# Kernel tuning notes

Measured on AMD Instinct MI355X. Metric: run time of the kernel, lower is better.

Reference implementation:

```python
import jax, jax.numpy as jnp
import numpy as np

GAMMA = 1.0
EPS = 1e-8


def setup_inputs() -> dict:
    key = jax.random.key(0)
    k1, k2 = jax.random.split(key)
    inputs = jax.random.normal(k1, (16, 2048, 1024), dtype=jnp.float32)
    codebook = jax.random.normal(k2, (2048, 1024), dtype=jnp.float32)  # normal(1.0) init
    return {"inputs": inputs, "codebook": codebook}


def reference(inputs, codebook):
    # inputs: [B, T, D]; codebook: [K, D]
    features = jax.lax.stop_gradient(inputs)
    # similarity = sum over D of features[..., None, :] * codebook -> [B, T, K]
    similarity = jnp.einsum('btd,kd->btk', features, codebook)
    scores = jax.nn.softmax(similarity, axis=-1)  # [B, T, K]
    nn_idx = jnp.argmax(scores, axis=-1)  # [B, T]
    # one_hot(nn_idx) @ codebook == direct gather
    quantized = codebook[nn_idx]  # [B, T, D]
    quantized = quantized - jnp.mean(quantized, axis=-1, keepdims=True)
    quantized = quantized / jnp.linalg.norm(quantized, axis=-1, keepdims=True)
    # entropy loss
    flat = scores.reshape(-1, scores.shape[-1])  # [B*T, K]
    h_clust = -jnp.mean(jnp.sum(flat * jnp.log2(flat + EPS), axis=-1))
    diversity = jnp.mean(flat, axis=0)  # [K]
    h_diversity = -jnp.sum(diversity * jnp.log2(diversity + EPS))
    loss = h_clust - GAMMA * h_diversity
    quantization_loss = jnp.full(scores.shape, loss)  # [B, T, K], scalar broadcast
    # straight-through estimator
    quantized = inputs + jax.lax.stop_gradient(quantized - inputs)
    return (quantized, quantization_loss, nn_idx, codebook)
```

## Files before the change

### kernel.cpp

```cpp
#include <hip/hip_runtime.h>
#include <math.h>

#define M_TOTAL 32768
#define D_DIM   1024
#define K_DIM   2048

#define OUT0_OFF 0ULL
#define OUT1_OFF 33554432ULL
#define OUT2_OFF 100663296ULL
#define OUT3_OFF 100696064ULL

typedef _Float16 f16x4 __attribute__((ext_vector_type(4)));
typedef _Float16 f16x8 __attribute__((ext_vector_type(8)));
typedef float    f32x4 __attribute__((ext_vector_type(4)));

#define STR_(x) #x
#define STR(x) STR_(x)
#define WAITVM(N) asm volatile("s_waitcnt vmcnt(" STR(N) ")" ::: "memory")

__device__ __forceinline__ void async_copy16(void* lds, const void* g) {
    __builtin_amdgcn_global_load_lds(
        (const __attribute__((address_space(1))) unsigned int*)g,
        (__attribute__((address_space(3))) unsigned int*)lds, 16, 0, 0);
}

__global__ __launch_bounds__(256) void convcb_kernel(const float* __restrict__ C,
                                                     _Float16* __restrict__ ch,
                                                     _Float16* __restrict__ cl) {
    const int i = blockIdx.x * 256 + threadIdx.x;
    const float4 c = ((const float4*)C)[i];
    f16x4 h, l;
    h.x = (_Float16)c.x; l.x = (_Float16)(c.x - (float)h.x);
    h.y = (_Float16)c.y; l.y = (_Float16)(c.y - (float)h.y);
    h.z = (_Float16)c.z; l.z = (_Float16)(c.z - (float)h.z);
    h.w = (_Float16)c.w; l.w = (_Float16)(c.w - (float)h.w);
    ((f16x4*)ch)[i] = h;
    ((f16x4*)cl)[i] = l;
}

__global__ __launch_bounds__(256) void convx_kernel(const float* __restrict__ X,
                                                    _Float16* __restrict__ xh) {
    const size_t i = (size_t)blockIdx.x * 256 + threadIdx.x;
    const float4 a = ((const float4*)X)[i];
    f16x4 h;
    h.x = (_Float16)a.x; h.y = (_Float16)a.y;
    h.z = (_Float16)a.z; h.w = (_Float16)a.w;
    ((f16x4*)xh)[i] = h;
}

__device__ __forceinline__ void loadA4(f16x8* a, const _Float16* Ab, int wm, int fr, int fq, int kh) {
#pragma unroll
    for (int mi = 0; mi < 4; mi++) {
        const int row = wm + mi * 16 + fr;
        a[mi] = *(const f16x8*)(Ab + kh * 8192 + row * 32 + (fq ^ ((row >> 1) & 3)) * 8);
    }
}
__device__ __forceinline__ void loadB4(f16x8* b, const _Float16* Bb, int wn, int fr, int fq, int kh) {
#pragma unroll
    for (int ni = 0; ni < 4; ni++) {
        const int row = wn + ni * 16 + fr;
        b[ni] = *(const f16x8*)(Bb + kh * 4096 + row * 32 + (fq ^ ((row >> 1) & 3)) * 8);
    }
}

__global__ __launch_bounds__(512) void gemm_kernel(const _Float16* __restrict__ XH,
                                                   const _Float16* __restrict__ CH,
                                                   const _Float16* __restrict__ CL,
                                                   float* __restrict__ S) {
    __shared__ _Float16 lds[65536];
    _Float16* const A0  = lds;
    _Float16* const Bh0 = lds + 16384;
    _Float16* const Bl0 = lds + 24576;
    _Float16* const A1  = lds + 32768;
    _Float16* const Bh1 = lds + 49152;
    _Float16* const Bl1 = lds + 57344;

    const int tid  = threadIdx.x;
    const int lane = tid & 63;
    const int wave = tid >> 6;

    const int bq  = blockIdx.x;
    const int xcd = bq & 7;
    const int idx = bq >> 3;
    const int m0 = (xcd * 16 + (idx >> 4)) * 256;
    const int n0 = (idx & 15) * 128;

    const int wm = (wave & 3) * 64;
    const int wn = (wave >> 2) * 64;
    const int fr = lane & 15;
    const int fq = lane >> 4;

    size_t aoff[2][2]; int alds[2][2];
#pragma unroll
    for (int e = 0; e < 2; e++) {
        const int U = (wave * 2 + e) * 64 + lane;
        const int row = U >> 2;
#pragma unroll
        for (int kh = 0; kh < 2; kh++) {
            aoff[e][kh] = (size_t)(m0 + row) * D_DIM + (size_t)(kh * 4 + ((U & 3) ^ ((row >> 1) & 3))) * 8;
            alds[e][kh] = kh * 8192 + (wave * 2 + e) * 512;
        }
    }
    size_t boff[2]; int blds[2];
    {
        const int U = wave * 64 + lane;
        const int row = U >> 2;
#pragma unroll
        for (int kh = 0; kh < 2; kh++) {
            boff[kh] = (size_t)(n0 + row) * D_DIM + (size_t)(kh * 4 + ((U & 3) ^ ((row >> 1) & 3))) * 8;
            blds[kh] = kh * 4096 + wave * 512;
        }
    }

#define STAGE_A(Abuf, KH, kb) do {                                                        \
    async_copy16((void*)((Abuf) + alds[0][KH]), (const void*)(XH + aoff[0][KH] + (kb)));  \
    async_copy16((void*)((Abuf) + alds[1][KH]), (const void*)(XH + aoff[1][KH] + (kb)));  \
} while (0)
#define STAGE_BH(Bbuf, KH, kb) async_copy16((void*)((Bbuf) + blds[KH]), (const void*)(CH + boff[KH] + (kb)))
#define STAGE_BL(Bbuf, KH, kb) async_copy16((void*)((Bbuf) + blds[KH]), (const void*)(CL + boff[KH] + (kb)))

#define PH_MFMA() do {                                                                    \
    __builtin_amdgcn_s_barrier();                                                         \
    asm volatile("s_waitcnt lgkmcnt(0)" ::: "memory");                                    \
    __builtin_amdgcn_sched_barrier(0);                                                    \
    __builtin_amdgcn_s_setprio(1);                                                        \
    _Pragma("unroll")                                                                     \
    for (int mi = 0; mi < 4; mi++) {                                                      \
        _Pragma("unroll")                                                                 \
        for (int ni = 0; ni < 4; ni++)                                                    \
            acc[mi][ni] = __builtin_amdgcn_mfma_f32_16x16x32_f16(a[mi], b[ni], acc[mi][ni], 0, 0, 0); \
    }                                                                                     \
    __builtin_amdgcn_s_setprio(0);                                                        \
    __builtin_amdgcn_s_barrier();                                                         \
} while (0)

    f32x4 acc[4][4];
#pragma unroll
    for (int mi = 0; mi < 4; mi++)
#pragma unroll
        for (int ni = 0; ni < 4; ni++) {
            acc[mi][ni].x = 0.f; acc[mi][ni].y = 0.f;
            acc[mi][ni].z = 0.f; acc[mi][ni].w = 0.f;
        }

    f16x8 a[4], b[4];

    STAGE_A(A0, 0, 0); STAGE_BH(Bh0, 0, 0);
    STAGE_BL(Bl0, 0, 0);
    STAGE_A(A0, 1, 0); STAGE_BH(Bh0, 1, 0);
    STAGE_BL(Bl0, 1, 0);
    WAITVM(5);
    __builtin_amdgcn_s_barrier();

    for (int t = 0; t < 15; t++) {
        _Float16* const Ac  = (t & 1) ? A1 : A0;
        _Float16* const Bhc = (t & 1) ? Bh1 : Bh0;
        _Float16* const Blc = (t & 1) ? Bl1 : Bl0;
        _Float16* const An  = (t & 1) ? A0 : A1;
        _Float16* const Bhn = (t & 1) ? Bh0 : Bh1;
        _Float16* const Bln = (t & 1) ? Bl0 : Bl1;
        const size_t kb = (size_t)(t + 1) * 64;

        loadA4(a, Ac, wm, fr, fq, 0);
        loadB4(b, Bhc, wn, fr, fq, 0);
        STAGE_A(An, 0, kb); STAGE_BH(Bhn, 0, kb);
        WAITVM(7);
        PH_MFMA();
        loadB4(b, Blc, wn, fr, fq, 0);
        STAGE_BL(Bln, 0, kb);
        WAITVM(5);
        PH_MFMA();
        loadA4(a, Ac, wm, fr, fq, 1);
        loadB4(b, Bhc, wn, fr, fq, 1);
        STAGE_A(An, 1, kb); STAGE_BH(Bhn, 1, kb);
        WAITVM(7);
        PH_MFMA();
        loadB4(b, Blc, wn, fr, fq, 1);
        STAGE_BL(Bln, 1, kb);
        WAITVM(5);
        PH_MFMA();
    }

    loadA4(a, A1, wm, fr, fq, 0);
    loadB4(b, Bh1, wn, fr, fq, 0);
    WAITVM(4);
    PH_MFMA();
    loadB4(b, Bl1, wn, fr, fq, 0);
    WAITVM(1);
    PH_MFMA();
    loadA4(a, A1, wm, fr, fq, 1);
    loadB4(b, Bh1, wn, fr, fq, 1);
    WAITVM(0);
    PH_MFMA();
    loadB4(b, Bl1, wn, fr, fq, 1);
    __builtin_amdgcn_s_barrier();
    asm volatile("s_waitcnt lgkmcnt(0)" ::: "memory");
    __builtin_amdgcn_sched_barrier(0);
#pragma unroll
    for (int mi = 0; mi < 4; mi++)
#pragma unroll
        for (int ni = 0; ni < 4; ni++)
            acc[mi][ni] = __builtin_amdgcn_mfma_f32_16x16x32_f16(a[mi], b[ni], acc[mi][ni], 0, 0, 0);

#pragma unroll
    for (int mi = 0; mi < 4; mi++)
#pragma unroll
        for (int r = 0; r < 4; r++) {
            float* dst = S + (size_t)(m0 + wm + mi * 16 + fq * 4 + r) * K_DIM + n0 + wn;
#pragma unroll
            for (int ni = 0; ni < 4; ni++) dst[ni * 16 + fr] = acc[mi][ni][r];
        }
#undef STAGE_A
#undef STAGE_BH
#undef STAGE_BL
#undef PH_MFMA
}

#define MARGIN 0.125f
__global__ __launch_bounds__(256) void rowstats_kernel(const float* __restrict__ S,
                                                       int* __restrict__ cnt,
                                                       int* __restrict__ cand,
                                                       float* __restrict__ div_acc,
                                                       float* __restrict__ hclust_acc) {
    __shared__ float sdiv[K_DIM];
    const int tid = threadIdx.x;
    for (int k = tid; k < K_DIM; k += 256) sdiv[k] = 0.0f;
    __syncthreads();

    const int lane = tid & 63;
    const int wave = tid >> 6;

    float dreg[32];
#pragma unroll
    for (int j = 0; j < 32; j++) dreg[j] = 0.0f;
    float ent_acc = 0.0f;

    for (int r8 = 0; r8 < 8; r8++) {
        const int row = blockIdx.x * 32 + wave * 8 + r8;
        const float* srow = S + (size_t)row * K_DIM;

        float v[32];
#pragma unroll
        for (int j = 0; j < 32; j++) v[j] = srow[lane + 64 * j];

        float m = v[0];
#pragma unroll
        for (int j = 1; j < 32; j++) m = fmaxf(m, v[j]);
        for (int off = 32; off > 0; off >>= 1) m = fmaxf(m, __shfl_xor(m, off, 64));

        const float thresh = m - MARGIN;
#pragma unroll
        for (int j = 0; j < 32; j++) {
            if (v[j] > thresh) {
                const int slot = atomicAdd(&cnt[row], 1);
                if (slot < 8) cand[row * 8 + slot] = lane + 64 * j;
            }
        }

        float Z = 0.0f;
#pragma unroll
        for (int j = 0; j < 32; j++) {
            v[j] = __expf(v[j] - m);
            Z += v[j];
        }
        for (int off = 32; off > 0; off >>= 1) Z += __shfl_xor(Z, off, 64);
        const float invZ = 1.0f / Z;

#pragma unroll
        for (int j = 0; j < 32; j++) {
            const float p = v[j] * invZ;
            dreg[j] += p;
            ent_acc += p * __log2f(p + 1e-8f);
        }
    }

#pragma unroll
    for (int j = 0; j < 32; j++) atomicAdd(&sdiv[lane + 64 * j], dreg[j]);
    for (int off = 32; off > 0; off >>= 1) ent_acc += __shfl_xor(ent_acc, off, 64);
    if (lane == 0) atomicAdd(hclust_acc, ent_acc);
    __syncthreads();

    for (int k = tid; k < K_DIM; k += 256) atomicAdd(&div_acc[k], sdiv[k]);
}

__global__ __launch_bounds__(256) void refineq_kernel(const float* __restrict__ X,
                                                      const float* __restrict__ C,
                                                      const int* __restrict__ cnt,
                                                      const int* __restrict__ cand,
                                                      float* __restrict__ nn_out,
                                                      float* __restrict__ out0) {
    const int tid = threadIdx.x;
    const int lane = tid & 63;
    const int wave = tid >> 6;
    const int row = blockIdx.x * 4 + wave;

    const int n = min(cnt[row], 8);
    const float* x = X + (size_t)row * D_DIM;

    float4 xv[4];
#pragma unroll
    for (int q = 0; q < 4; q++) xv[q] = *(const float4*)(x + lane * 4 + 256 * q);

    double bestv = -1.0e300;
    int besti = 0x7fffffff;
    for (int c = 0; c < n; c++) {
        const int idx = cand[row * 8 + c];
        const float* cb = C + (size_t)idx * D_DIM;
        double s = 0.0;
#pragma unroll
        for (int q = 0; q < 4; q++) {
            const float4 cv = *(const float4*)(cb + lane * 4 + 256 * q);
            s += (double)xv[q].x * cv.x + (double)xv[q].y * cv.y +
                 (double)xv[q].z * cv.z + (double)xv[q].w * cv.w;
        }
        for (int off = 32; off > 0; off >>= 1) s += __shfl_xor(s, off, 64);
        if (s > bestv || (s == bestv && idx < besti)) { bestv = s; besti = idx; }
    }
    if (lane == 0) nn_out[row] = (float)besti;

    const float* c = C + (size_t)besti * D_DIM;
    float4 v[4];
    float sum = 0.0f;
#pragma unroll
    for (int q = 0; q < 4; q++) {
        v[q] = *(const float4*)(c + lane * 4 + 256 * q);
        sum += v[q].x + v[q].y + v[q].z + v[q].w;
    }
    for (int off = 32; off > 0; off >>= 1) sum += __shfl_xor(sum, off, 64);
    const float mean = sum * (1.0f / 1024.0f);

    float ss = 0.0f;
#pragma unroll
    for (int q = 0; q < 4; q++) {
        v[q].x -= mean; v[q].y -= mean; v[q].z -= mean; v[q].w -= mean;
        ss += v[q].x * v[q].x + v[q].y * v[q].y + v[q].z * v[q].z + v[q].w * v[q].w;
    }
    for (int off = 32; off > 0; off >>= 1) ss += __shfl_xor(ss, off, 64);
    const float inv = 1.0f / sqrtf(ss);

    float* o = out0 + (size_t)row * D_DIM;
#pragma unroll
    for (int q = 0; q < 4; q++) {
        float4 w = v[q];
        w.x *= inv; w.y *= inv; w.z *= inv; w.w *= inv;
        *(float4*)(o + lane * 4 + 256 * q) = w;
    }
}

__global__ __launch_bounds__(256) void finalize_kernel(const float* __restrict__ div_acc,
                                                       const float* __restrict__ hclust_acc,
                                                       float* __restrict__ loss_out) {
    __shared__ float red[256];
    const int tid = threadIdx.x;
    float sum = 0.0f;
    for (int k = tid; k < K_DIM; k += 256) {
        const float d = div_acc[k] * (1.0f / 32768.0f);
        sum += d * __log2f(d + 1e-8f);
    }
    red[tid] = sum;
    __syncthreads();
    for (int s = 128; s > 0; s >>= 1) {
        if (tid < s) red[tid] += red[tid + s];
        __syncthreads();
    }
    if (tid == 0) {
        const float h_clust = -hclust_acc[0] * (1.0f / 32768.0f);
        const float h_div = -red[0];
        loss_out[0] = h_clust - 1.0f * h_div;
    }
}

__global__ __launch_bounds__(256) void fill_kernel(float* __restrict__ out1,
                                                   const float* __restrict__ loss_ptr) {
    const float v = loss_ptr[0];
    const float4 f = make_float4(v, v, v, v);
    float4* o = (float4*)out1;
    const size_t stride = (size_t)gridDim.x * blockDim.x;
    for (size_t i = (size_t)blockIdx.x * blockDim.x + threadIdx.x; i < 16777216ULL; i += stride)
        o[i] = f;
}

__global__ __launch_bounds__(256) void copycb_kernel(const float* __restrict__ C,
                                                     float* __restrict__ out3) {
    const size_t i = (size_t)blockIdx.x * 256 + threadIdx.x;
    if (i < 524288ULL) ((float4*)out3)[i] = ((const float4*)C)[i];
}

extern "C" void kernel_launch(void* const* d_in, const int* in_sizes, int n_in,
                              void* d_out, int out_size, void* d_ws, size_t ws_size,
                              hipStream_t stream) {
    const float* X = (const float*)d_in[0];
    const float* C = (const float*)d_in[1];
    float* out = (float*)d_out;

    char* scratch = (char*)d_out;
    _Float16* CH  = (_Float16*)(scratch);
    _Float16* CL  = (_Float16*)(scratch + (4 << 20));
    _Float16* XH  = (_Float16*)(scratch + (16 << 20));

    char* s3 = (char*)(out + OUT3_OFF);
    int* cand      = (int*)s3;
    int* cnt       = (int*)(s3 + (1 << 20));
    float* div_acc = (float*)(s3 + (1 << 20) + (128 << 10));
    float* hclust  = div_acc + 2048;
    float* loss    = div_acc + 2049;

    float* S = out + OUT1_OFF;

    hipMemsetAsync(s3 + (1 << 20), 0, (128 << 10) + 8192 + 16, stream);

    convcb_kernel<<<2048, 256, 0, stream>>>(C, CH, CL);

    convx_kernel<<<32768, 256, 0, stream>>>(X, XH);

    gemm_kernel<<<2048, 512, 0, stream>>>(XH, CH, CL, S);

    rowstats_kernel<<<M_TOTAL / 32, 256, 0, stream>>>(S, cnt, cand, div_acc, hclust);

    refineq_kernel<<<M_TOTAL / 4, 256, 0, stream>>>(X, C, cnt, cand,
                                                    out + OUT2_OFF, out + OUT0_OFF);

    finalize_kernel<<<1, 256, 0, stream>>>(div_acc, hclust, loss);

    fill_kernel<<<8192, 256, 0, stream>>>(out + OUT1_OFF, loss);

    copycb_kernel<<<2048, 256, 0, stream>>>(C, out + OUT3_OFF);
}
```

Before: 951.8 us.

## Deepen GEMM K-phases and fuse row stats with candidate refinement

The GEMM main loop now loads both k-halves of a 64-wide K slice at once and issues 32 MFMAs per phase, so each iteration has two barrier phases instead of four. It also adds a two-blocks-per-CU launch bound. The row-stats and refine kernels are merged so candidate counts and indices stay in shared memory, which removes the global atomics, the cand/cnt buffers, their memset, and one kernel launch. In exchange the GEMM needs more registers for the larger fragments, which may conflict with the occupancy hint, and the fused kernel runs refinement serially after the stats pass with fewer waves per row.

```diff
diff --git a/kernel.cpp b/kernel.cpp
--- a/kernel.cpp
+++ b/kernel.cpp
@@ -48,25 +48,29 @@
     ((f16x4*)xh)[i] = h;
 }
 
-__device__ __forceinline__ void loadA4(f16x8* a, const _Float16* Ab, int wm, int fr, int fq, int kh) {
-#pragma unroll
-    for (int mi = 0; mi < 4; mi++) {
-        const int row = wm + mi * 16 + fr;
-        a[mi] = *(const f16x8*)(Ab + kh * 8192 + row * 32 + (fq ^ ((row >> 1) & 3)) * 8);
-    }
-}
-__device__ __forceinline__ void loadB4(f16x8* b, const _Float16* Bb, int wn, int fr, int fq, int kh) {
-#pragma unroll
-    for (int ni = 0; ni < 4; ni++) {
-        const int row = wn + ni * 16 + fr;
-        b[ni] = *(const f16x8*)(Bb + kh * 4096 + row * 32 + (fq ^ ((row >> 1) & 3)) * 8);
-    }
-}
-
-__global__ __launch_bounds__(512) void gemm_kernel(const _Float16* __restrict__ XH,
-                                                   const _Float16* __restrict__ CH,
-                                                   const _Float16* __restrict__ CL,
-                                                   float* __restrict__ S) {
+__device__ __forceinline__ void loadA8(f16x8* a, const _Float16* Ab, int wm, int fr, int fq) {
+#pragma unroll
+    for (int kh = 0; kh < 2; kh++)
+#pragma unroll
+        for (int mi = 0; mi < 4; mi++) {
+            const int row = wm + mi * 16 + fr;
+            a[kh * 4 + mi] = *(const f16x8*)(Ab + kh * 8192 + row * 32 + (fq ^ ((row >> 1) & 3)) * 8);
+        }
+}
+__device__ __forceinline__ void loadB8(f16x8* b, const _Float16* Bb, int wn, int fr, int fq) {
+#pragma unroll
+    for (int kh = 0; kh < 2; kh++)
+#pragma unroll
+        for (int ni = 0; ni < 4; ni++) {
+            const int row = wn + ni * 16 + fr;
+            b[kh * 4 + ni] = *(const f16x8*)(Bb + kh * 4096 + row * 32 + (fq ^ ((row >> 1) & 3)) * 8);
+        }
+}
+
+__global__ __launch_bounds__(512, 2) void gemm_kernel(const _Float16* __restrict__ XH,
+                                                      const _Float16* __restrict__ CH,
+                                                      const _Float16* __restrict__ CL,
+                                                      float* __restrict__ S) {
     __shared__ _Float16 lds[65536];
     _Float16* const A0  = lds;
     _Float16* const Bh0 = lds + 16384;
@@ -112,26 +116,35 @@
         }
     }
 
-#define STAGE_A(Abuf, KH, kb) do {                                                        \
-    async_copy16((void*)((Abuf) + alds[0][KH]), (const void*)(XH + aoff[0][KH] + (kb)));  \
-    async_copy16((void*)((Abuf) + alds[1][KH]), (const void*)(XH + aoff[1][KH] + (kb)));  \
+#define STAGE_C0(Abuf, Bbuf, kb) do {                                                       \
+    async_copy16((void*)((Abuf) + alds[0][0]), (const void*)(XH + aoff[0][0] + (kb)));      \
+    async_copy16((void*)((Abuf) + alds[1][0]), (const void*)(XH + aoff[1][0] + (kb)));      \
+    async_copy16((void*)((Abuf) + alds[0][1]), (const void*)(XH + aoff[0][1] + (kb)));      \
+    async_copy16((void*)((Abuf) + alds[1][1]), (const void*)(XH + aoff[1][1] + (kb)));      \
+    async_copy16((void*)((Bbuf) + blds[0]),    (const void*)(CH + boff[0] + (kb)));         \
+    async_copy16((void*)((Bbuf) + blds[1]),    (const void*)(CH + boff[1] + (kb)));         \
 } while (0)
-#define STAGE_BH(Bbuf, KH, kb) async_copy16((void*)((Bbuf) + blds[KH]), (const void*)(CH + boff[KH] + (kb)))
-#define STAGE_BL(Bbuf, KH, kb) async_copy16((void*)((Bbuf) + blds[KH]), (const void*)(CL + boff[KH] + (kb)))
-
-#define PH_MFMA() do {                                                                    \
-    __builtin_amdgcn_s_barrier();                                                         \
-    asm volatile("s_waitcnt lgkmcnt(0)" ::: "memory");                                    \
-    __builtin_amdgcn_sched_barrier(0);                                                    \
-    __builtin_amdgcn_s_setprio(1);                                                        \
-    _Pragma("unroll")                                                                     \
-    for (int mi = 0; mi < 4; mi++) {                                                      \
-        _Pragma("unroll")                                                                 \
-        for (int ni = 0; ni < 4; ni++)                                                    \
-            acc[mi][ni] = __builtin_amdgcn_mfma_f32_16x16x32_f16(a[mi], b[ni], acc[mi][ni], 0, 0, 0); \
-    }                                                                                     \
-    __builtin_amdgcn_s_setprio(0);                                                        \
-    __builtin_amdgcn_s_barrier();                                                         \
+#define STAGE_C1(Bbuf, kb) do {                                                             \
+    async_copy16((void*)((Bbuf) + blds[0]),    (const void*)(CL + boff[0] + (kb)));         \
+    async_copy16((void*)((Bbuf) + blds[1]),    (const void*)(CL + boff[1] + (kb)));         \
+} while (0)
+
+#define PH32() do {                                                                         \
+    __builtin_amdgcn_s_barrier();                                                           \
+    asm volatile("s_waitcnt lgkmcnt(0)" ::: "memory");                                      \
+    __builtin_amdgcn_sched_barrier(0);                                                      \
+    __builtin_amdgcn_s_setprio(1);                                                          \
+    _Pragma("unroll")                                                                       \
+    for (int kh = 0; kh < 2; kh++) {                                                        \
+        _Pragma("unroll")                                                                   \
+        for (int mi = 0; mi < 4; mi++) {                                                    \
+            _Pragma("unroll")                                                               \
+            for (int ni = 0; ni < 4; ni++)                                                  \
+                acc[mi][ni] = __builtin_amdgcn_mfma_f32_16x16x32_f16(a[kh * 4 + mi], b[kh * 4 + ni], acc[mi][ni], 0, 0, 0); \
+        }                                                                                   \
+    }                                                                                       \
+    __builtin_amdgcn_s_setprio(0);                                                          \
+    __builtin_amdgcn_s_barrier();                                                           \
 } while (0)
 
     f32x4 acc[4][4];
@@ -143,13 +156,11 @@
             acc[mi][ni].z = 0.f; acc[mi][ni].w = 0.f;
         }
 
-    f16x8 a[4], b[4];
-
-    STAGE_A(A0, 0, 0); STAGE_BH(Bh0, 0, 0);
-    STAGE_BL(Bl0, 0, 0);
-    STAGE_A(A0, 1, 0); STAGE_BH(Bh0, 1, 0);
-    STAGE_BL(Bl0, 1, 0);
-    WAITVM(5);
+    f16x8 a[8], b[8];
+
+    STAGE_C0(A0, Bh0, 0);
+    STAGE_C1(Bl0, 0);
+    WAITVM(2);
     __builtin_amdgcn_s_barrier();
 
     for (int t = 0; t < 15; t++) {
@@ -161,46 +172,31 @@
         _Float16* const Bln = (t & 1) ? Bl0 : Bl1;
         const size_t kb = (size_t)(t + 1) * 64;
 
-        loadA4(a, Ac, wm, fr, fq, 0);
-        loadB4(b, Bhc, wn, fr, fq, 0);
-        STAGE_A(An, 0, kb); STAGE_BH(Bhn, 0, kb);
-        WAITVM(7);
-        PH_MFMA();
-        loadB4(b, Blc, wn, fr, fq, 0);
-        STAGE_BL(Bln, 0, kb);
-        WAITVM(5);
-        PH_MFMA();
-        loadA4(a, Ac, wm, fr, fq, 1);
-        loadB4(b, Bhc, wn, fr, fq, 1);
-        STAGE_A(An, 1, kb); STAGE_BH(Bhn, 1, kb);
-        WAITVM(7);
-        PH_MFMA();
-        loadB4(b, Blc, wn, fr, fq, 1);
-        STAGE_BL(Bln, 1, kb);
-        WAITVM(5);
-        PH_MFMA();
-    }
-
-    loadA4(a, A1, wm, fr, fq, 0);
-    loadB4(b, Bh1, wn, fr, fq, 0);
-    WAITVM(4);
-    PH_MFMA();
-    loadB4(b, Bl1, wn, fr, fq, 0);
-    WAITVM(1);
-    PH_MFMA();
-    loadA4(a, A1, wm, fr, fq, 1);
-    loadB4(b, Bh1, wn, fr, fq, 1);
+        loadA8(a, Ac, wm, fr, fq);
+        loadB8(b, Bhc, wn, fr, fq);
+        STAGE_C0(An, Bhn, kb);
+        WAITVM(6);
+        PH32();
+        loadB8(b, Blc, wn, fr, fq);
+        STAGE_C1(Bln, kb);
+        WAITVM(2);
+        PH32();
+    }
+
+    loadA8(a, A1, wm, fr, fq);
+    loadB8(b, Bh1, wn, fr, fq);
     WAITVM(0);
-    PH_MFMA();
-    loadB4(b, Bl1, wn, fr, fq, 1);
-    __builtin_amdgcn_s_barrier();
+    PH32();
+    loadB8(b, Bl1, wn, fr, fq);
     asm volatile("s_waitcnt lgkmcnt(0)" ::: "memory");
     __builtin_amdgcn_sched_barrier(0);
 #pragma unroll
-    for (int mi = 0; mi < 4; mi++)
-#pragma unroll
-        for (int ni = 0; ni < 4; ni++)
-            acc[mi][ni] = __builtin_amdgcn_mfma_f32_16x16x32_f16(a[mi], b[ni], acc[mi][ni], 0, 0, 0);
+    for (int kh = 0; kh < 2; kh++)
+#pragma unroll
+        for (int mi = 0; mi < 4; mi++)
+#pragma unroll
+            for (int ni = 0; ni < 4; ni++)
+                acc[mi][ni] = __builtin_amdgcn_mfma_f32_16x16x32_f16(a[kh * 4 + mi], b[kh * 4 + ni], acc[mi][ni], 0, 0, 0);
 
 #pragma unroll
     for (int mi = 0; mi < 4; mi++)
@@ -210,21 +206,25 @@
 #pragma unroll
             for (int ni = 0; ni < 4; ni++) dst[ni * 16 + fr] = acc[mi][ni][r];
         }
-#undef STAGE_A
-#undef STAGE_BH
-#undef STAGE_BL
-#undef PH_MFMA
+#undef STAGE_C0
+#undef STAGE_C1
+#undef PH32
 }
 
 #define MARGIN 0.125f
-__global__ __launch_bounds__(256) void rowstats_kernel(const float* __restrict__ S,
-                                                       int* __restrict__ cnt,
-                                                       int* __restrict__ cand,
+__global__ __launch_bounds__(256) void statsref_kernel(const float* __restrict__ S,
+                                                       const float* __restrict__ X,
+                                                       const float* __restrict__ C,
                                                        float* __restrict__ div_acc,
-                                                       float* __restrict__ hclust_acc) {
+                                                       float* __restrict__ hclust_acc,
+                                                       float* __restrict__ nn_out,
+                                                       float* __restrict__ out0) {
     __shared__ float sdiv[K_DIM];
+    __shared__ int scnt[32];
+    __shared__ int scand[32][8];
     const int tid = threadIdx.x;
     for (int k = tid; k < K_DIM; k += 256) sdiv[k] = 0.0f;
+    if (tid < 32) scnt[tid] = 0;
     __syncthreads();
 
     const int lane = tid & 63;
@@ -236,7 +236,8 @@
     float ent_acc = 0.0f;
 
     for (int r8 = 0; r8 < 8; r8++) {
-        const int row = blockIdx.x * 32 + wave * 8 + r8;
+        const int lr = wave * 8 + r8;
+        const int row = blockIdx.x * 32 + lr;
         const float* srow = S + (size_t)row * K_DIM;
 
         float v[32];
@@ -252,8 +253,8 @@
 #pragma unroll
         for (int j = 0; j < 32; j++) {
             if (v[j] > thresh) {
-                const int slot = atomicAdd(&cnt[row], 1);
-                if (slot < 8) cand[row * 8 + slot] = lane + 64 * j;
+                const int slot = atomicAdd(&scnt[lr], 1);
+                if (slot < 8) scand[lr][slot] = lane + 64 * j;
             }
         }
 
@@ -281,69 +282,61 @@
     __syncthreads();
 
     for (int k = tid; k < K_DIM; k += 256) atomicAdd(&div_acc[k], sdiv[k]);
-}
-
-__global__ __launch_bounds__(256) void refineq_kernel(const float* __restrict__ X,
-                                                      const float* __restrict__ C,
-                                                      const int* __restrict__ cnt,
-                                                      const int* __restrict__ cand,
-                                                      float* __restrict__ nn_out,
-                                                      float* __restrict__ out0) {
-    const int tid = threadIdx.x;
-    const int lane = tid & 63;
-    const int wave = tid >> 6;
-    const int row = blockIdx.x * 4 + wave;
-
-    const int n = min(cnt[row], 8);
-    const float* x = X + (size_t)row * D_DIM;
-
-    float4 xv[4];
-#pragma unroll
-    for (int q = 0; q < 4; q++) xv[q] = *(const float4*)(x + lane * 4 + 256 * q);
-
-    double bestv = -1.0e300;
-    int besti = 0x7fffffff;
-    for (int c = 0; c < n; c++) {
-        const int idx = cand[row * 8 + c];
-        const float* cb = C + (size_t)idx * D_DIM;
-        double s = 0.0;
+
+    for (int r8 = 0; r8 < 8; r8++) {
+        const int lr = wave * 8 + r8;
+        const int row = blockIdx.x * 32 + lr;
+        const int n = min(scnt[lr], 8);
+        const float* x = X + (size_t)row * D_DIM;
+
+        float4 xv[4];
+#pragma unroll
+        for (int q = 0; q < 4; q++) xv[q] = *(const float4*)(x + lane * 4 + 256 * q);
+
+        double bestv = -1.0e300;
+        int besti = 0x7fffffff;
+        for (int c = 0; c < n; c++) {
+            const int cidx = scand[lr][c];
+            const float* cb = C + (size_t)cidx * D_DIM;
+            double s = 0.0;
+#pragma unroll
+            for (int q = 0; q < 4; q++) {
+                const float4 cv = *(const float4*)(cb + lane * 4 + 256 * q);
+                s += (double)xv[q].x * cv.x + (double)xv[q].y * cv.y +
+                     (double)xv[q].z * cv.z + (double)xv[q].w * cv.w;
+            }
+            for (int off = 32; off > 0; off >>= 1) s += __shfl_xor(s, off, 64);
+            if (s > bestv || (s == bestv && cidx < besti)) { bestv = s; besti = cidx; }
+        }
+        if (lane == 0) nn_out[row] = (float)besti;
+
+        const float* c = C + (size_t)besti * D_DIM;
+        float4 v[4];
+        float sum = 0.0f;
 #pragma unroll
         for (int q = 0; q < 4; q++) {
-            const float4 cv = *(const float4*)(cb + lane * 4 + 256 * q);
-            s += (double)xv[q].x * cv.x + (double)xv[q].y * cv.y +
-                 (double)xv[q].z * cv.z + (double)xv[q].w * cv.w;
-        }
-        for (int off = 32; off > 0; off >>= 1) s += __shfl_xor(s, off, 64);
-        if (s > bestv || (s == bestv && idx < besti)) { bestv = s; besti = idx; }
-    }
-    if (lane == 0) nn_out[row] = (float)besti;
-
-    const float* c = C + (size_t)besti * D_DIM;
-    float4 v[4];
-    float sum = 0.0f;
-#pragma unroll
-    for (int q = 0; q < 4; q++) {
-        v[q] = *(const float4*)(c + lane * 4 + 256 * q);
-        sum += v[q].x + v[q].y + v[q].z + v[q].w;
-    }
-    for (int off = 32; off > 0; off >>= 1) sum += __shfl_xor(sum, off, 64);
-    const float mean = sum * (1.0f / 1024.0f);
-
-    float ss = 0.0f;
-#pragma unroll
-    for (int q = 0; q < 4; q++) {
-        v[q].x -= mean; v[q].y -= mean; v[q].z -= mean; v[q].w -= mean;
-        ss += v[q].x * v[q].x + v[q].y * v[q].y + v[q].z * v[q].z + v[q].w * v[q].w;
-    }
-    for (int off = 32; off > 0; off >>= 1) ss += __shfl_xor(ss, off, 64);
-    const float inv = 1.0f / sqrtf(ss);
-
-    float* o = out0 + (size_t)row * D_DIM;
-#pragma unroll
-    for (int q = 0; q < 4; q++) {
-        float4 w = v[q];
-        w.x *= inv; w.y *= inv; w.z *= inv; w.w *= inv;
-        *(float4*)(o + lane * 4 + 256 * q) = w;
+            v[q] = *(const float4*)(c + lane * 4 + 256 * q);
+            sum += v[q].x + v[q].y + v[q].z + v[q].w;
+        }
+        for (int off = 32; off > 0; off >>= 1) sum += __shfl_xor(sum, off, 64);
+        const float mean = sum * (1.0f / 1024.0f);
+
+        float ss = 0.0f;
+#pragma unroll
+        for (int q = 0; q < 4; q++) {
+            v[q].x -= mean; v[q].y -= mean; v[q].z -= mean; v[q].w -= mean;
+            ss += v[q].x * v[q].x + v[q].y * v[q].y + v[q].z * v[q].z + v[q].w * v[q].w;
+        }
+        for (int off = 32; off > 0; off >>= 1) ss += __shfl_xor(ss, off, 64);
+        const float inv = 1.0f / sqrtf(ss);
+
+        float* o = out0 + (size_t)row * D_DIM;
+#pragma unroll
+        for (int q = 0; q < 4; q++) {
+            float4 w = v[q];
+            w.x *= inv; w.y *= inv; w.z *= inv; w.w *= inv;
+            *(float4*)(o + lane * 4 + 256 * q) = w;
+        }
     }
 }
 
@@ -399,15 +392,13 @@
     _Float16* XH  = (_Float16*)(scratch + (16 << 20));
 
     char* s3 = (char*)(out + OUT3_OFF);
-    int* cand      = (int*)s3;
-    int* cnt       = (int*)(s3 + (1 << 20));
-    float* div_acc = (float*)(s3 + (1 << 20) + (128 << 10));
+    float* div_acc = (float*)s3;
     float* hclust  = div_acc + 2048;
     float* loss    = div_acc + 2049;
 
     float* S = out + OUT1_OFF;
 
-    hipMemsetAsync(s3 + (1 << 20), 0, (128 << 10) + 8192 + 16, stream);
+    hipMemsetAsync(s3, 0, 8192 + 16, stream);
 
     convcb_kernel<<<2048, 256, 0, stream>>>(C, CH, CL);
 
@@ -415,10 +406,8 @@
 
     gemm_kernel<<<2048, 512, 0, stream>>>(XH, CH, CL, S);
 
-    rowstats_kernel<<<M_TOTAL / 32, 256, 0, stream>>>(S, cnt, cand, div_acc, hclust);
-
-    refineq_kernel<<<M_TOTAL / 4, 256, 0, stream>>>(X, C, cnt, cand,
-                                                    out + OUT2_OFF, out + OUT0_OFF);
+    statsref_kernel<<<M_TOTAL / 32, 256, 0, stream>>>(S, X, C, div_acc, hclust,
+                                                      out + OUT2_OFF, out + OUT0_OFF);
 
     finalize_kernel<<<1, 256, 0, stream>>>(div_acc, hclust, loss);
 
```

Result: faster. 913.3 us (-4.1%).
